# Kernel tuning notes

Hardware: AMD Instinct MI355X
Metric: run time of the kernel (lower is better)

## Reference

```python
import jax, jax.numpy as jnp
import numpy as np

N, DIM, HEADS, NS, KSP = 16384, 192, 6, 16, 16


def _forward(knn_idx, p, x, W_qkv, W_proj, b_proj, prop_W, prop_b, gA_W, gA_b, gB_W, gB_b,
             gC_W, gC_b, pos_W1, pos_b1, pos_gamma, pos_beta, pos_W2, pos_b2, kn,
             de_W1, de_b1, de_W2, de_b2, kp_W, kp_b, fus_W, fus_b):
    n, d = x.shape
    ns = knn_idx.shape[1]
    D = d // HEADS
    scale = D ** -0.5
    knn_xyz = p[knn_idx]                                  # [n,ns,3] irregular gather
    p_r = knn_xyz - p[:, None, :]                         # relative coords
    x_knn = x[knn_idx]                                    # [n,ns,d] irregular gather
    # PropagateLayer: rel-pos conditioned neighbor message + residual
    msg = jax.nn.relu(jnp.concatenate([x_knn, p_r], -1) @ prop_W + prop_b)
    x = x + msg.mean(1)
    # local polar representation
    dist_r = jnp.sqrt(jnp.sum(p_r * p_r, -1, keepdims=True) + 1e-12)   # [n,ns,1]
    geo_rep = jnp.concatenate([p_r, knn_xyz, jnp.broadcast_to(p[:, None, :], p_r.shape)], -1).mean(1)  # [n,9]
    geo_dis = dist_r.max(1)                               # [n,1]
    vol = (dist_r.mean() / (dist_r.max() + 1e-8)).reshape(1, 1)
    geo_rep = geo_rep @ gA_W + gA_b
    geo_dis = geo_dis @ gB_W + gB_b
    vol = vol @ gC_W + gC_b                               # [1,d] broadcast over n
    # keypoint distance features + attention pooling (KeyPointAttention)
    dist = jnp.sqrt(jnp.sum((p[:, None, :] - kn[None, :, :]) ** 2, -1) + 1e-12)  # [n,KSP]
    df = jax.nn.relu(dist[..., None] @ de_W1 + de_b1) @ de_W2 + de_b2            # [n,KSP,d]
    sc = jax.nn.softmax(df @ kp_W + kp_b, axis=1)
    dist_feat = (sc * df).sum(1)                          # [n,d]
    # FeatureFusion
    x = (x + geo_rep + geo_dis + vol + dist_feat) @ fus_W + fus_b
    # QueryGroup(local=True): window features + intra-window pairwise rel coords
    wx = x[knn_idx]                                       # [n,ns,d] irregular gather
    pos = (knn_xyz[:, None, :, :] - knn_xyz[:, :, None, :]).reshape(n, ns, ns * 3)  # [n,ns,48]

    def posi(i):  # Linear -> BatchNorm1d(dim) over (batch, window) -> ReLU -> Linear
        h = pos @ pos_W1[i] + pos_b1[i]                   # [n,ns,d]
        mu = h.mean((0, 1))
        var = h.var((0, 1))
        h = (h - mu) * jax.lax.rsqrt(var + 1e-5) * pos_gamma[i] + pos_beta[i]
        return jax.nn.relu(h) @ pos_W2[i] + pos_b2[i]

    pq, pk, pv = posi(0), posi(1), posi(2)
    q, k, v = jnp.split(wx @ W_qkv, 3, -1)

    def heads(t):
        return t.reshape(n, ns, HEADS, D).transpose(0, 2, 1, 3)  # [n,h,ns,D]

    q, k, v, pq, pk, pv = map(heads, (q, k, v, pq, pk, pv))
    dots = (jnp.einsum('nhid,nhjd->nhij', q, k)
            + jnp.einsum('nhid,nhjd->nhij', q, pq)
            + jnp.einsum('nhid,nhjd->nhij', k, pk))      # fused positional bias scores
    attn = jax.nn.softmax(dots * scale, -1)
    out = jnp.einsum('nhij,nhjd->nhid', attn, v + pv)
    out = out.transpose(0, 2, 1, 3).reshape(n, ns, d)[:, 0, :]   # take window center
    return out @ W_proj + b_proj


def setup_inputs() -> dict:
    key = jax.random.key(0)
    ks = jax.random.split(key, 20)
    d, s = DIM, 0.05
    rn = lambda i, shape: jax.random.normal(ks[i], shape, dtype=jnp.float32)
    return {
        'p': rn(0, (N, 3)),
        'x': rn(1, (N, d)),
        'knn_idx': jax.random.randint(ks[2], (N, NS), 0, N),
        'W_qkv': rn(3, (d, 3 * d)) * s,
        'W_proj': rn(4, (d, d)) * s,
        'b_proj': jnp.zeros((d,)),
        'prop_W': rn(5, (d + 3, d)) * s,
        'prop_b': jnp.zeros((d,)),
        'gA_W': rn(6, (9, d)) * s, 'gA_b': jnp.zeros((d,)),
        'gB_W': rn(7, (1, d)) * s, 'gB_b': jnp.zeros((d,)),
        'gC_W': rn(8, (1, d)) * s, 'gC_b': jnp.zeros((d,)),
        'pos_W1': rn(9, (3, NS * 3, d)) * s, 'pos_b1': jnp.zeros((3, d)),
        'pos_gamma': jnp.ones((3, d)), 'pos_beta': jnp.zeros((3, d)),
        'pos_W2': rn(10, (3, d, d)) * s, 'pos_b2': jnp.zeros((3, d)),
        'kn': rn(11, (KSP, 3)),
        'de_W1': rn(12, (1, d // 4)) * s, 'de_b1': jnp.zeros((d // 4,)),
        'de_W2': rn(13, (d // 4, d)) * s, 'de_b2': jnp.zeros((d,)),
        'kp_W': rn(14, (d, 1)) * s, 'kp_b': jnp.zeros((1,)),
        'fus_W': rn(15, (d, d)) * s, 'fus_b': jnp.zeros((d,)),
    }


def reference(p, x, knn_idx, W_qkv, W_proj, b_proj, prop_W, prop_b, gA_W, gA_b, gB_W, gB_b,
              gC_W, gC_b, pos_W1, pos_b1, pos_gamma, pos_beta, pos_W2, pos_b2, kn,
              de_W1, de_b1, de_W2, de_b2, kp_W, kp_b, fus_W, fus_b):
    return _forward(knn_idx, p, x, W_qkv, W_proj, b_proj, prop_W, prop_b, gA_W, gA_b,
                    gB_W, gB_b, gC_W, gC_b, pos_W1, pos_b1, pos_gamma, pos_beta,
                    pos_W2, pos_b2, kn, de_W1, de_b1, de_W2, de_b2, kp_W, kp_b, fus_W, fus_b)
```

## Files before the change

kernel.cpp:

```cpp
#include <hip/hip_runtime.h>
#include <math.h>

#define NP 16384
#define DD 192
#define NS 16
#define KSPN 16
#define MTOT (NP*NS)

typedef unsigned short ushort_t;
typedef __attribute__((ext_vector_type(8))) short short8;
typedef __attribute__((ext_vector_type(4))) float f32x4;

__device__ __forceinline__ ushort_t f2bf(float f) {
    union { float f; unsigned int u; } v; v.f = f;
    return (ushort_t)((v.u + 0x7FFFu + ((v.u >> 16) & 1u)) >> 16);
}
__device__ __forceinline__ float bf2f(ushort_t u) {
    return __uint_as_float(((unsigned int)u) << 16);
}

#define WS_KNN   0
#define WS_PR    (WS_KNN + NP*48)
#define WS_GEO9  (WS_PR + MTOT*3)
#define WS_GDIS  (WS_GEO9 + NP*9)
#define WS_STATS (WS_GDIS + NP)
#define WS_VOLV  (WS_STATS + 2512)
#define WS_AB    (WS_VOLV + DD)
#define WS_X1    (WS_AB + 1152)
#define WS_U     (WS_X1 + NP*DD)
#define WS_X2    (WS_U + NP*DD)
#define WS_QKV   (WS_X2 + NP*DD)
#define WS_SC    (WS_QKV + NP*576)
#define WS_ATTN  (WS_SC + NP*DD)
#define WS_W2T   (WS_ATTN + NP*96)
#define WS_PROPWT (WS_W2T + 36864)
#define WS_QKVT  (WS_PROPWT + 18432)
#define WS_FUSWT (WS_QKVT + 55296)
#define WS_PROJWT (WS_FUSWT + 18432)
#define WS_W1T   (WS_PROJWT + 18432)
#define WS_DEW2T (WS_W1T + 18432)
#define WS_XB    WS_SC
#define WS_UB    WS_ATTN
#define WS_X2B   WS_X2
#define WS_CTRB  WS_U

__global__ __launch_bounds__(256) void k_init(float* __restrict__ ws) {
    int t = blockIdx.x * 256 + threadIdx.x;
    if (t < 2512) ws[WS_STATS + t] = 0.f;
}

__global__ __launch_bounds__(256) void k_w2t(const float* __restrict__ posW2,
                                             float* __restrict__ ws) {
    int e = blockIdx.x*256 + threadIdx.x;
    int c = e / DD, kk = e - c*DD;
    ws[WS_W2T + e] = posW2[(size_t)(2*DD + kk)*DD + c];
}

__global__ __launch_bounds__(256) void k_prep(
    const float* __restrict__ propW, const float* __restrict__ Wqkv,
    const float* __restrict__ fusW, const float* __restrict__ Wproj,
    const float* __restrict__ posW1, const float* __restrict__ deW2,
    float* __restrict__ ws)
{
    int e = blockIdx.x*256 + threadIdx.x;
    ushort_t* pwt = (ushort_t*)(ws + WS_PROPWT);
    ushort_t* qkt = (ushort_t*)(ws + WS_QKVT);
    ushort_t* fwt = (ushort_t*)(ws + WS_FUSWT);
    ushort_t* pjt = (ushort_t*)(ws + WS_PROJWT);
    ushort_t* w1t = (ushort_t*)(ws + WS_W1T);
    ushort_t* dwt = (ushort_t*)(ws + WS_DEW2T);
    if (e < 36864) {
        int n = e/192, k = e - n*192;
        pwt[e] = f2bf(propW[(size_t)k*192 + n]);
    } else if (e < 147456) {
        int r = e - 36864; int n = r/192, k = r - n*192;
        qkt[r] = f2bf(Wqkv[(size_t)k*576 + n]);
    } else if (e < 184320) {
        int r = e - 147456; int n = r/192, k = r - n*192;
        fwt[r] = f2bf(fusW[(size_t)k*192 + n]);
    } else if (e < 221184) {
        int r = e - 184320; int n = r/192, k = r - n*192;
        pjt[r] = f2bf(Wproj[(size_t)k*192 + n]);
    } else if (e < 258048) {
        int r = e - 221184;
        int i = r / 12288, rem = r - i*12288;
        int n = rem / 64, k = rem - n*64;
        w1t[r] = (k < 48) ? f2bf(posW1[(size_t)(i*48 + k)*DD + n]) : (ushort_t)0;
    } else if (e < 270336) {
        int r = e - 258048;
        int n = r / 64, k = r - n*64;
        dwt[r] = (k < 48) ? f2bf(deW2[(size_t)k*DD + n]) : (ushort_t)0;
    }
}

__global__ __launch_bounds__(256) void k_castx(const float* __restrict__ x,
                                               float* __restrict__ ws) {
    int e = blockIdx.x*256 + threadIdx.x;
    ((ushort_t*)(ws + WS_XB))[e] = f2bf(x[e]);
}

__global__ __launch_bounds__(256) void k1a_geom(
    const float* __restrict__ p, const int* __restrict__ knn,
    float* __restrict__ ws)
{
    __shared__ float red[32];
    const int t = threadIdx.x;
    const int w = t >> 4, u = t & 15;
    const int n = blockIdx.x*16 + w;
    const int idx = knn[n*NS + u];
    const float X0 = p[idx*3+0], X1 = p[idx*3+1], X2 = p[idx*3+2];
    const float pn0 = p[n*3+0], pn1 = p[n*3+1], pn2 = p[n*3+2];
    ws[WS_KNN + (size_t)n*48 + u*3 + 0] = X0;
    ws[WS_KNN + (size_t)n*48 + u*3 + 1] = X1;
    ws[WS_KNN + (size_t)n*48 + u*3 + 2] = X2;
    const float dx = X0-pn0, dy = X1-pn1, dz = X2-pn2;
    ws[WS_PR + (size_t)(n*NS+u)*3 + 0] = dx;
    ws[WS_PR + (size_t)(n*NS+u)*3 + 1] = dy;
    ws[WS_PR + (size_t)(n*NS+u)*3 + 2] = dz;
    const float dist = sqrtf(dx*dx + dy*dy + dz*dz + 1e-12f);
    float dmx = dist, dsm = dist, S0 = X0, S1 = X1, S2 = X2;
    #pragma unroll
    for (int off = 1; off < 16; off <<= 1) {
        dmx = fmaxf(dmx, __shfl_xor(dmx, off, 16));
        dsm += __shfl_xor(dsm, off, 16);
        S0 += __shfl_xor(S0, off, 16);
        S1 += __shfl_xor(S1, off, 16);
        S2 += __shfl_xor(S2, off, 16);
    }
    if (u == 0) {
        ws[WS_GDIS + n] = dmx;
        float m0 = S0*(1.f/16.f), m1 = S1*(1.f/16.f), m2 = S2*(1.f/16.f);
        float* g = ws + WS_GEO9 + (size_t)n*9;
        g[0] = m0-pn0; g[1] = m1-pn1; g[2] = m2-pn2;
        g[3] = m0; g[4] = m1; g[5] = m2;
        g[6] = pn0; g[7] = pn1; g[8] = pn2;
        red[w] = dsm; red[16+w] = dmx;
    }
    __syncthreads();
    if (t == 0) {
        float ds = 0.f, dm = 0.f;
        #pragma unroll
        for (int i = 0; i < 16; ++i) { ds += red[i]; dm = fmaxf(dm, red[16+i]); }
        atomicAdd(&ws[WS_STATS + 0], ds);
        atomicMax((int*)(ws + WS_STATS + 1), __float_as_int(dm));
    }
}

__global__ __launch_bounds__(256) void k1b_stats(float* __restrict__ ws)
{
    __shared__ float Xs[128][48];
    __shared__ float Ss[128][3];
    __shared__ float a3p[9][16];
    const int t = threadIdx.x;
    const int c0 = blockIdx.x * 128;
    for (int e = t; e < 1536; e += 256) {
        int r = e/12, q = e%12;
        *(float4*)&Xs[r][q*4] = *(const float4*)(ws + WS_KNN + (size_t)(c0+r)*48 + q*4);
    }
    __syncthreads();
    if (t < 128) {
        float s0 = 0.f, s1 = 0.f, s2 = 0.f;
        #pragma unroll
        for (int j = 0; j < 16; ++j) { s0 += Xs[t][3*j]; s1 += Xs[t][3*j+1]; s2 += Xs[t][3*j+2]; }
        Ss[t][0] = s0; Ss[t][1] = s1; Ss[t][2] = s2;
    }
    __syncthreads();
    {
        float acc[9];
        #pragma unroll
        for (int q = 0; q < 9; ++q) acc[q] = 0.f;
        for (int i = 0; i < 128; ++i) {
            int e = t;
            #pragma unroll
            for (int q = 0; q < 9; ++q) {
                int a = e/48, b = e%48;
                acc[q] += Xs[i][a] * Xs[i][b];
                e += 256;
            }
        }
        int e = t;
        #pragma unroll
        for (int q = 0; q < 9; ++q) { atomicAdd(&ws[WS_STATS + 50 + e], acc[q]); e += 256; }
    }
    if (t < 144) {
        int a = t/3, d = t%3;
        float s = 0.f;
        for (int i = 0; i < 128; ++i) s += Xs[i][a] * Ss[i][d];
        atomicAdd(&ws[WS_STATS + 2354 + t], s);
    }
    if (t < 144) {
        int q = t >> 4, part = t & 15;
        int d = q/3, e2 = q%3;
        float s = 0.f;
        for (int i = part*8; i < part*8 + 8; ++i) {
            #pragma unroll
            for (int j = 0; j < 16; ++j) s += Xs[i][3*j+d] * Xs[i][3*j+e2];
        }
        a3p[q][part] = s;
    }
    if (t < 48) {
        float s = 0.f;
        for (int i = 0; i < 128; ++i) s += Xs[i][t];
        atomicAdd(&ws[WS_STATS + 2 + t], s);
    }
    if (t < 3) {
        float s = 0.f;
        for (int i = 0; i < 128; ++i) s += Ss[i][t];
        atomicAdd(&ws[WS_STATS + 2507 + t], s);
    }
    __syncthreads();
    if (t < 9) {
        float s = 0.f;
        #pragma unroll
        for (int i = 0; i < 16; ++i) s += a3p[t][i];
        atomicAdd(&ws[WS_STATS + 2498 + t], s);
    }
}

__global__ __launch_bounds__(256) void k2_fold(
    const float* __restrict__ posW1, const float* __restrict__ posB1,
    const float* __restrict__ gamma, const float* __restrict__ beta,
    const float* __restrict__ gCW, const float* __restrict__ gCb,
    float* __restrict__ ws)
{
    __shared__ float M2n[48][48];
    __shared__ float pmean[48];
    __shared__ float Wc[48][193];
    const int t = threadIdx.x;
    const int i = blockIdx.x;
    for (int e = t; e < 2304; e += 256) {
        int a = e/48, b = e%48, ad = a%3, bd = b%3;
        float v = 16.f*ws[WS_STATS + 50 + e]
                - ws[WS_STATS + 2354 + a*3 + bd]
                - ws[WS_STATS + 2354 + b*3 + ad]
                + ws[WS_STATS + 2498 + ad*3 + bd];
        M2n[a][b] = v * (1.f/(float)MTOT);
    }
    if (t < 48) pmean[t] = (16.f*ws[WS_STATS + 2 + t] - ws[WS_STATS + 2507 + t%3])
                           * (1.f/(float)MTOT);
    if (t < DD) {
        for (int k = 0; k < 48; ++k) Wc[k][t] = posW1[(size_t)(i*48 + k)*DD + t];
    }
    __syncthreads();
    if (i == 0 && t < DD) {
        float dsum = ws[WS_STATS + 0];
        float dmax = __int_as_float(((const int*)(ws + WS_STATS))[1]);
        float vol = (dsum * (1.f/(float)MTOT)) / (dmax + 1e-8f);
        ws[WS_VOLV + t] = vol * gCW[t] + gCb[t];
    }
    if (t < DD) {
        float mu0 = 0.f;
        #pragma unroll 8
        for (int k = 0; k < 48; ++k) mu0 += pmean[k] * Wc[k][t];
        float e2 = 0.f;
        for (int a2 = 0; a2 < 48; ++a2) {
            float inner = 0.f;
            #pragma unroll 8
            for (int b2 = 0; b2 < 48; ++b2) inner += M2n[a2][b2] * Wc[b2][t];
            e2 += Wc[a2][t] * inner;
        }
        float var = fmaxf(e2 - mu0*mu0, 0.f);
        float as = rsqrtf(var + 1e-5f) * gamma[i*DD + t];
        ws[WS_AB + i*DD + t]       = as;
        ws[WS_AB + 576 + i*DD + t] = beta[i*DD + t] - mu0 * as;
    }
}

__global__ __launch_bounds__(256) void k_prop_mfma(
    const float* __restrict__ x, const int* __restrict__ knn,
    const float* __restrict__ propW, const float* __restrict__ propB,
    float* __restrict__ ws)
{
    __shared__ ushort_t As[64*40];
    __shared__ ushort_t Bs[192*40];
    __shared__ float prs[64*3];
    __shared__ float W3[3*192];
    __shared__ int idx64[64];
    const int t = threadIdx.x;
    const int mbase = blockIdx.x * 64;
    const ushort_t* xb = (const ushort_t*)(ws + WS_XB);
    const ushort_t* pwt = (const ushort_t*)(ws + WS_PROPWT);
    if (t < 64) idx64[t] = knn[mbase + t];
    for (int e = t; e < 576; e += 256) W3[e] = propW[(size_t)(192 + e/192)*DD + (e % 192)];
    for (int e = t; e < 192; e += 256) prs[e] = ws[WS_PR + (size_t)mbase*3 + e];
    const int wave = t >> 6, lane = t & 63, m = lane & 15, quad = lane >> 4;
    f32x4 acc[12];
    #pragma unroll
    for (int nt = 0; nt < 12; ++nt) acc[nt] = (f32x4){0.f,0.f,0.f,0.f};
    for (int ks = 0; ks < 6; ++ks) {
        const int k0 = ks*32;
        __syncthreads();
        {   int r = t >> 2, seg = t & 3;
            *(uint4*)&As[r*40 + seg*8] = *(const uint4*)(xb + (size_t)idx64[r]*192 + k0 + seg*8);
        }
        for (int e = t; e < 768; e += 256) {
            int n = e >> 2, seg = e & 3;
            *(uint4*)&Bs[n*40 + seg*8] = *(const uint4*)(pwt + (size_t)n*192 + k0 + seg*8);
        }
        __syncthreads();
        short8 a = *(const short8*)&As[(wave*16 + m)*40 + quad*8];
        #pragma unroll
        for (int nt = 0; nt < 12; ++nt) {
            short8 b = *(const short8*)&Bs[(nt*16 + m)*40 + quad*8];
            acc[nt] = __builtin_amdgcn_mfma_f32_16x16x32_bf16(a, b, acc[nt], 0, 0, 0);
        }
    }
    const int n = blockIdx.x*4 + wave;
    #pragma unroll
    for (int nt = 0; nt < 12; ++nt) {
        int col = nt*16 + m;
        float bv = propB[col];
        float w0 = W3[col], w1 = W3[192 + col], w2 = W3[384 + col];
        float s = 0.f;
        #pragma unroll
        for (int reg = 0; reg < 4; ++reg) {
            int j = wave*16 + quad*4 + reg;
            float v = acc[nt][reg] + prs[j*3+0]*w0 + prs[j*3+1]*w1 + prs[j*3+2]*w2 + bv;
            s += fmaxf(v, 0.f);
        }
        s += __shfl_xor(s, 16);
        s += __shfl_xor(s, 32);
        if (quad == 0)
            ws[WS_X1 + (size_t)n*DD + col] = x[(size_t)n*DD + col] + s * (1.f/16.f);
    }
}

__global__ __launch_bounds__(256) void gemm_mfma(
    const ushort_t* __restrict__ A, const ushort_t* __restrict__ Bt,
    const float* __restrict__ bias, float* __restrict__ Cf,
    ushort_t* __restrict__ Cb, int N)
{
    __shared__ ushort_t As[64*40];
    __shared__ ushort_t Bs[64*40];
    const int t = threadIdx.x;
    const int wave = t >> 6, lane = t & 63, m = lane & 15, quad = lane >> 4;
    const int rowBase = blockIdx.x * 64, colBase = blockIdx.y * 64;
    f32x4 acc[4];
    #pragma unroll
    for (int nt = 0; nt < 4; ++nt) acc[nt] = (f32x4){0.f,0.f,0.f,0.f};
    for (int ks = 0; ks < 6; ++ks) {
        __syncthreads();
        {   int r = t >> 2, seg = t & 3;
            *(uint4*)&As[r*40 + seg*8] = *(const uint4*)(A + (size_t)(rowBase + r)*192 + ks*32 + seg*8);
            *(uint4*)&Bs[r*40 + seg*8] = *(const uint4*)(Bt + (size_t)(colBase + r)*192 + ks*32 + seg*8);
        }
        __syncthreads();
        short8 a = *(const short8*)&As[(wave*16 + m)*40 + quad*8];
        #pragma unroll
        for (int nt = 0; nt < 4; ++nt) {
            short8 b = *(const short8*)&Bs[(nt*16 + m)*40 + quad*8];
            acc[nt] = __builtin_amdgcn_mfma_f32_16x16x32_bf16(a, b, acc[nt], 0, 0, 0);
        }
    }
    #pragma unroll
    for (int nt = 0; nt < 4; ++nt) {
        int col = colBase + nt*16 + m;
        float bv = bias ? bias[col] : 0.f;
        #pragma unroll
        for (int reg = 0; reg < 4; ++reg) {
            int row = rowBase + wave*16 + quad*4 + reg;
            float v = acc[nt][reg] + bv;
            if (Cf) Cf[(size_t)row*N + col] = v;
            else    Cb[(size_t)row*N + col] = f2bf(v);
        }
    }
}

__global__ __launch_bounds__(256) void k3a(
    const float* __restrict__ p, const float* __restrict__ kn,
    const float* __restrict__ deW1, const float* __restrict__ deB1,
    const float* __restrict__ deB2, const float* __restrict__ kpW,
    const float* __restrict__ gAW, const float* __restrict__ gAb,
    const float* __restrict__ gBW, const float* __restrict__ gBb,
    float* __restrict__ ws)
{
    __shared__ ushort_t fb[128*72];
    __shared__ float kds[8][16];
    __shared__ float w1s[48], b1s[48];
    __shared__ float dfeat[8][192];
    ushort_t* ub = (ushort_t*)(ws + WS_UB);
    const int t = threadIdx.x;
    const int nb = blockIdx.x * 8;
    if (t < 48) { w1s[t] = deW1[t]; b1s[t] = deB1[t]; }
    if (t < 128) {
        int w = t >> 4, kp = t & 15;
        float dx = p[(nb+w)*3+0]-kn[kp*3+0];
        float dy = p[(nb+w)*3+1]-kn[kp*3+1];
        float dz = p[(nb+w)*3+2]-kn[kp*3+2];
        kds[w][kp] = sqrtf(dx*dx + dy*dy + dz*dz + 1e-12f);
    }
    __syncthreads();
    for (int e = t; e < 128*64; e += 256) {
        int j = e >> 6, k = e & 63;
        float v = (k < 48) ? fmaxf(kds[j>>4][j&15]*w1s[k] + b1s[k], 0.f) : 0.f;
        fb[j*72 + k] = f2bf(v);
    }
    __syncthreads();
    const int wave = t >> 6, lane = t & 63, m = lane & 15, quad = lane >> 4;
    const ushort_t* dwt = (const ushort_t*)(ws + WS_DEW2T);
    short8 afr[2][2];
    #pragma unroll
    for (int mt = 0; mt < 2; ++mt)
        #pragma unroll
        for (int ks = 0; ks < 2; ++ks)
            afr[mt][ks] = *(const short8*)&fb[((wave*2 + mt)*16 + m)*72 + ks*32 + quad*8];
    float df[2][12][4];
    float sc[2][4];
    #pragma unroll
    for (int mt = 0; mt < 2; ++mt)
        #pragma unroll
        for (int reg = 0; reg < 4; ++reg) sc[mt][reg] = 0.f;
    for (int nt = 0; nt < 12; ++nt) {
        f32x4 acc0 = (f32x4){0.f,0.f,0.f,0.f};
        f32x4 acc1 = (f32x4){0.f,0.f,0.f,0.f};
        #pragma unroll
        for (int ks = 0; ks < 2; ++ks) {
            short8 b = *(const short8*)(dwt + ((size_t)(nt*16 + m)*64 + ks*32 + quad*8));
            acc0 = __builtin_amdgcn_mfma_f32_16x16x32_bf16(afr[0][ks], b, acc0, 0, 0, 0);
            acc1 = __builtin_amdgcn_mfma_f32_16x16x32_bf16(afr[1][ks], b, acc1, 0, 0, 0);
        }
        int col = nt*16 + m;
        float b2 = deB2[col], kw = kpW[col];
        #pragma unroll
        for (int reg = 0; reg < 4; ++reg) {
            float d0 = acc0[reg] + b2, d1 = acc1[reg] + b2;
            df[0][nt][reg] = d0; df[1][nt][reg] = d1;
            sc[0][reg] += d0*kw; sc[1][reg] += d1*kw;
        }
    }
    #pragma unroll
    for (int mt = 0; mt < 2; ++mt)
        #pragma unroll
        for (int reg = 0; reg < 4; ++reg) {
            float v = sc[mt][reg];
            v += __shfl_xor(v, 1, 16); v += __shfl_xor(v, 2, 16);
            v += __shfl_xor(v, 4, 16); v += __shfl_xor(v, 8, 16);
            sc[mt][reg] = v;
        }
    float wgt[2][4];
    #pragma unroll
    for (int mt = 0; mt < 2; ++mt) {
        float mx = fmaxf(fmaxf(sc[mt][0], sc[mt][1]), fmaxf(sc[mt][2], sc[mt][3]));
        mx = fmaxf(mx, __shfl_xor(mx, 16));
        mx = fmaxf(mx, __shfl_xor(mx, 32));
        float sm = 0.f;
        #pragma unroll
        for (int reg = 0; reg < 4; ++reg) { wgt[mt][reg] = expf(sc[mt][reg] - mx); sm += wgt[mt][reg]; }
        sm += __shfl_xor(sm, 16);
        sm += __shfl_xor(sm, 32);
        float inv = 1.f / sm;
        #pragma unroll
        for (int reg = 0; reg < 4; ++reg) wgt[mt][reg] *= inv;
    }
    for (int nt = 0; nt < 12; ++nt) {
        int col = nt*16 + m;
        #pragma unroll
        for (int mt = 0; mt < 2; ++mt) {
            float s = 0.f;
            #pragma unroll
            for (int reg = 0; reg < 4; ++reg) s += wgt[mt][reg] * df[mt][nt][reg];
            s += __shfl_xor(s, 16);
            s += __shfl_xor(s, 32);
            if (quad == 0) dfeat[wave*2 + mt][col] = s;
        }
    }
    __syncthreads();
    if (t < DD) {
        for (int w = 0; w < 8; ++w) {
            int n = nb + w;
            float uval = ws[WS_X1 + (size_t)n*DD + t] + gAb[t] + gBb[t]
                       + ws[WS_VOLV + t] + dfeat[w][t];
            uval += ws[WS_GDIS + n] * gBW[t];
            #pragma unroll
            for (int kk = 0; kk < 9; ++kk) uval += ws[WS_GEO9 + (size_t)n*9 + kk] * gAW[kk*DD + t];
            ub[(size_t)n*DD + t] = f2bf(uval);
        }
    }
}

__global__ __launch_bounds__(256) void k_attn_fused(
    const int* __restrict__ knn,
    const float* __restrict__ posW2, const float* __restrict__ posB2,
    float* __restrict__ ws)
{
    __shared__ ushort_t posb[128*72];
    __shared__ float rqs[8*6*192];
    __shared__ float qk[8*192];
    __shared__ float scb[8*192];
    __shared__ float dqk[8*96];
    __shared__ float attns[8*96];
    __shared__ float Xl[8][48];
    __shared__ int idxs[128];
    const int t = threadIdx.x;
    const int nb = blockIdx.x * 8;
    ushort_t* ctrb = (ushort_t*)(ws + WS_CTRB);
    const ushort_t* qkvb = (const ushort_t*)(ws + WS_QKV);
    if (t < 128) idxs[t] = knn[(nb + (t >> 4))*NS + (t & 15)];
    for (int e = t; e < 384; e += 256) {
        int w = e/48, k = e%48;
        Xl[w][k] = ws[WS_KNN + (size_t)(nb+w)*48 + k];
    }
    __syncthreads();
    for (int e = t; e < 128*64; e += 256) {
        int j = e >> 6, k = e & 63;
        int w = j >> 4, jl = j & 15;
        float v = (k < 48) ? (Xl[w][k] - Xl[w][jl*3 + (k % 3)]) : 0.f;
        posb[j*72 + k] = f2bf(v);
    }
    const int wave = t >> 6, lane = t & 63, m = lane & 15, quad = lane >> 4;
    const ushort_t* w1t = (const ushort_t*)(ws + WS_W1T);
    for (int i = 0; i < 2; ++i) {
        __syncthreads();
        for (int e = t; e < 8*192; e += 256) {
            int w = e/192, c = e%192;
            qk[e] = bf2f(qkvb[(size_t)idxs[w*16]*576 + i*192 + c]);
        }
        __syncthreads();
        if (t < 192) {
            const float* Wrow = posW2 + (size_t)i*DD*DD + (size_t)t*DD;
            for (int h = 0; h < 6; ++h) {
                float4 wr[8];
                #pragma unroll
                for (int q = 0; q < 8; ++q) wr[q] = *(const float4*)(Wrow + h*32 + q*4);
                float a[8];
                #pragma unroll
                for (int w = 0; w < 8; ++w) a[w] = 0.f;
                #pragma unroll
                for (int q = 0; q < 8; ++q) {
                    #pragma unroll
                    for (int d = 0; d < 4; ++d) {
                        float wv = (&wr[q].x)[d];
                        int c = h*32 + q*4 + d;
                        #pragma unroll
                        for (int w = 0; w < 8; ++w) a[w] += wv * qk[w*192 + c];
                    }
                }
                #pragma unroll
                for (int w = 0; w < 8; ++w) rqs[(w*6 + h)*192 + t] = a[w];
            }
        }
        __syncthreads();
        short8 afr[2][2];
        #pragma unroll
        for (int mt = 0; mt < 2; ++mt)
            #pragma unroll
            for (int ks = 0; ks < 2; ++ks)
                afr[mt][ks] = *(const short8*)&posb[((wave*2 + mt)*16 + m)*72 + ks*32 + quad*8];
        float s[48];
        #pragma unroll
        for (int e = 0; e < 48; ++e) s[e] = 0.f;
        for (int nt = 0; nt < 12; ++nt) {
            f32x4 acc0 = (f32x4){0.f,0.f,0.f,0.f};
            f32x4 acc1 = (f32x4){0.f,0.f,0.f,0.f};
            #pragma unroll
            for (int ks = 0; ks < 2; ++ks) {
                short8 b = *(const short8*)(w1t + ((size_t)(i*192 + nt*16 + m)*64 + ks*32 + quad*8));
                acc0 = __builtin_amdgcn_mfma_f32_16x16x32_bf16(afr[0][ks], b, acc0, 0, 0, 0);
                acc1 = __builtin_amdgcn_mfma_f32_16x16x32_bf16(afr[1][ks], b, acc1, 0, 0, 0);
            }
            int kk = nt*16 + m;
            float as = ws[WS_AB + i*DD + kk];
            float bb = ws[WS_AB + 576 + i*DD + kk];
            float h0[4], h1[4];
            #pragma unroll
            for (int reg = 0; reg < 4; ++reg) {
                h0[reg] = fmaxf(acc0[reg]*as + bb, 0.f);
                h1[reg] = fmaxf(acc1[reg]*as + bb, 0.f);
            }
            #pragma unroll
            for (int h = 0; h < 6; ++h) {
                float r0 = rqs[((wave*2 + 0)*6 + h)*192 + kk];
                float r1 = rqs[((wave*2 + 1)*6 + h)*192 + kk];
                #pragma unroll
                for (int reg = 0; reg < 4; ++reg) {
                    s[reg*6 + h]      += h0[reg]*r0;
                    s[24 + reg*6 + h] += h1[reg]*r1;
                }
            }
        }
        #pragma unroll
        for (int e = 0; e < 48; ++e) {
            float v = s[e];
            v += __shfl_xor(v, 1, 16); v += __shfl_xor(v, 2, 16);
            v += __shfl_xor(v, 4, 16); v += __shfl_xor(v, 8, 16);
            s[e] = v;
        }
        if (m == 0) {
            #pragma unroll
            for (int mt = 0; mt < 2; ++mt)
                #pragma unroll
                for (int reg = 0; reg < 4; ++reg) {
                    int w = wave*2 + mt, j = quad*4 + reg;
                    #pragma unroll
                    for (int h = 0; h < 6; ++h)
                        scb[w*192 + i*96 + h*16 + j] = s[mt*24 + reg*6 + h];
                }
        }
    }
    {
        const int w = t >> 5, r = t & 31, j = r >> 1, half = r & 1;
        const ushort_t* krow = qkvb + (size_t)idxs[w*16 + j]*576 + 192 + half*96;
        const ushort_t* qrow = qkvb + (size_t)idxs[w*16]*576 + half*96;
        float hd[3] = {0.f, 0.f, 0.f};
        #pragma unroll
        for (int q = 0; q < 12; ++q) {
            uint4 kv = *(const uint4*)(krow + q*8);
            uint4 qv = *(const uint4*)(qrow + q*8);
            float sv = 0.f;
            #pragma unroll
            for (int d = 0; d < 4; ++d) {
                unsigned int ku = (&kv.x)[d], qu = (&qv.x)[d];
                sv += __uint_as_float(ku << 16) * __uint_as_float(qu << 16);
                sv += __uint_as_float(ku & 0xffff0000u) * __uint_as_float(qu & 0xffff0000u);
            }
            hd[q >> 2] += sv;
        }
        dqk[w*96 + (half*3+0)*16 + j] = hd[0];
        dqk[w*96 + (half*3+1)*16 + j] = hd[1];
        dqk[w*96 + (half*3+2)*16 + j] = hd[2];
    }
    __syncthreads();
    {
        const float scale = 0.17677669529663687f;
        #pragma unroll
        for (int c = 0; c < 3; ++c) {
            int e = c*256 + t;
            int row = e >> 4, j = e & 15, w = row / 6, h = row % 6;
            float z = (dqk[e] + scb[w*192 + h*16 + j] + scb[w*192 + 96 + h*16 + j]) * scale;
            float mx = z;
            #pragma unroll
            for (int off = 1; off < 16; off <<= 1) mx = fmaxf(mx, __shfl_xor(mx, off, 16));
            float ex = expf(z - mx);
            float sm = ex;
            #pragma unroll
            for (int off = 1; off < 16; off <<= 1) sm += __shfl_xor(sm, off, 16);
            attns[w*96 + h*16 + j] = ex / sm;
        }
    }
    __syncthreads();
    float ctr1[8];
    if (t < DD) {
        const int h = t >> 5;
        #pragma unroll
        for (int w = 0; w < 8; ++w) {
            float sv = 0.f;
            #pragma unroll
            for (int j = 0; j < NS; ++j)
                sv += attns[w*96 + h*16 + j] * bf2f(qkvb[(size_t)idxs[w*16 + j]*576 + 384 + t]);
            ctr1[w] = sv;
        }
    }
    {
        float* wsum = rqs;
        const int w0 = wave*2, w1 = wave*2 + 1;
        short8 afr[2][2];
        #pragma unroll
        for (int mt = 0; mt < 2; ++mt)
            #pragma unroll
            for (int ks = 0; ks < 2; ++ks)
                afr[mt][ks] = *(const short8*)&posb[((wave*2 + mt)*16 + m)*72 + ks*32 + quad*8];
        for (int nt = 0; nt < 12; ++nt) {
            f32x4 acc0 = (f32x4){0.f,0.f,0.f,0.f};
            f32x4 acc1 = (f32x4){0.f,0.f,0.f,0.f};
            #pragma unroll
            for (int ks = 0; ks < 2; ++ks) {
                short8 b = *(const short8*)(w1t + ((size_t)(2*192 + nt*16 + m)*64 + ks*32 + quad*8));
                acc0 = __builtin_amdgcn_mfma_f32_16x16x32_bf16(afr[0][ks], b, acc0, 0, 0, 0);
                acc1 = __builtin_amdgcn_mfma_f32_16x16x32_bf16(afr[1][ks], b, acc1, 0, 0, 0);
            }
            int kk = nt*16 + m;
            float as = ws[WS_AB + 2*DD + kk];
            float bb = ws[WS_AB + 576 + 2*DD + kk];
            float h0[4], h1[4];
            #pragma unroll
            for (int reg = 0; reg < 4; ++reg) {
                h0[reg] = fmaxf(acc0[reg]*as + bb, 0.f);
                h1[reg] = fmaxf(acc1[reg]*as + bb, 0.f);
            }
            #pragma unroll
            for (int h = 0; h < 6; ++h) {
                float p0 = 0.f, p1 = 0.f;
                #pragma unroll
                for (int reg = 0; reg < 4; ++reg) {
                    int j = quad*4 + reg;
                    p0 += attns[w0*96 + h*16 + j] * h0[reg];
                    p1 += attns[w1*96 + h*16 + j] * h1[reg];
                }
                p0 += __shfl_xor(p0, 16); p0 += __shfl_xor(p0, 32);
                p1 += __shfl_xor(p1, 16); p1 += __shfl_xor(p1, 32);
                if (quad == 0) {
                    wsum[(w0*6 + h)*192 + kk] = p0;
                    wsum[(w1*6 + h)*192 + kk] = p1;
                }
            }
        }
    }
    __syncthreads();
    if (t < DD) {
        const float* wsum = rqs;
        const int h = t >> 5;
        float pvacc[8];
        #pragma unroll
        for (int w = 0; w < 8; ++w) pvacc[w] = 0.f;
        const float* wrow = ws + WS_W2T + (size_t)t*DD;
        for (int k4 = 0; k4 < 48; ++k4) {
            float4 wv = *(const float4*)(wrow + k4*4);
            #pragma unroll
            for (int w = 0; w < 8; ++w) {
                const float* av = &wsum[(w*6 + h)*192 + k4*4];
                pvacc[w] += av[0]*wv.x + av[1]*wv.y + av[2]*wv.z + av[3]*wv.w;
            }
        }
        float b2 = posB2[2*DD + t];
        #pragma unroll
        for (int w = 0; w < 8; ++w)
            ctrb[(size_t)(nb+w)*DD + t] = f2bf(ctr1[w] + pvacc[w] + b2);
    }
}

extern "C" void kernel_launch(void* const* d_in, const int* in_sizes, int n_in,
                              void* d_out, int out_size, void* d_ws, size_t ws_size,
                              hipStream_t stream)
{
    const float* p     = (const float*)d_in[0];
    const float* x     = (const float*)d_in[1];
    const int*   knn   = (const int*)  d_in[2];
    const float* Wqkv  = (const float*)d_in[3];
    const float* Wproj = (const float*)d_in[4];
    const float* bproj = (const float*)d_in[5];
    const float* propW = (const float*)d_in[6];
    const float* propB = (const float*)d_in[7];
    const float* gAW   = (const float*)d_in[8];
    const float* gAb   = (const float*)d_in[9];
    const float* gBW   = (const float*)d_in[10];
    const float* gBb   = (const float*)d_in[11];
    const float* gCW   = (const float*)d_in[12];
    const float* gCb   = (const float*)d_in[13];
    const float* posW1 = (const float*)d_in[14];
    const float* posB1 = (const float*)d_in[15];
    const float* gamma = (const float*)d_in[16];
    const float* beta  = (const float*)d_in[17];
    const float* posW2 = (const float*)d_in[18];
    const float* posB2 = (const float*)d_in[19];
    const float* kn    = (const float*)d_in[20];
    const float* deW1  = (const float*)d_in[21];
    const float* deB1  = (const float*)d_in[22];
    const float* deW2  = (const float*)d_in[23];
    const float* deB2  = (const float*)d_in[24];
    const float* kpW   = (const float*)d_in[25];
    const float* kpB   = (const float*)d_in[26];
    const float* fusW  = (const float*)d_in[27];
    const float* fusB  = (const float*)d_in[28];
    float* ws   = (float*)d_ws;
    float* outp = (float*)d_out;
    (void)kpB;

    hipLaunchKernelGGL(k_init, dim3(10), dim3(256), 0, stream, ws);
    hipLaunchKernelGGL(k_w2t, dim3(144), dim3(256), 0, stream, posW2, ws);
    hipLaunchKernelGGL(k_prep, dim3(1056), dim3(256), 0, stream,
                       propW, Wqkv, fusW, Wproj, posW1, deW2, ws);
    hipLaunchKernelGGL(k_castx, dim3(NP*DD/256), dim3(256), 0, stream, x, ws);
    hipLaunchKernelGGL(k1a_geom, dim3(NP/16), dim3(256), 0, stream, p, knn, ws);
    hipLaunchKernelGGL(k1b_stats, dim3(NP/128), dim3(256), 0, stream, ws);
    hipLaunchKernelGGL(k2_fold, dim3(3), dim3(256), 0, stream,
                       posW1, posB1, gamma, beta, gCW, gCb, ws);
    hipLaunchKernelGGL(k_prop_mfma, dim3(MTOT/64), dim3(256), 0, stream,
                       x, knn, propW, propB, ws);
    hipLaunchKernelGGL(k3a, dim3(NP/8), dim3(256), 0, stream,
                       p, kn, deW1, deB1, deB2, kpW, gAW, gAb, gBW, gBb, ws);
    hipLaunchKernelGGL(gemm_mfma, dim3(NP/64, 3), dim3(256), 0, stream,
                       (const ushort_t*)(ws + WS_UB), (const ushort_t*)(ws + WS_FUSWT),
                       fusB, (float*)nullptr, (ushort_t*)(ws + WS_X2B), DD);
    hipLaunchKernelGGL(gemm_mfma, dim3(NP/64, 9), dim3(256), 0, stream,
                       (const ushort_t*)(ws + WS_X2B), (const ushort_t*)(ws + WS_QKVT),
                       (const float*)nullptr, (float*)nullptr,
                       (ushort_t*)(ws + WS_QKV), 576);
    hipLaunchKernelGGL(k_attn_fused, dim3(NP/8), dim3(256), 0, stream,
                       knn, posW2, posB2, ws);
    hipLaunchKernelGGL(gemm_mfma, dim3(NP/64, 3), dim3(256), 0, stream,
                       (const ushort_t*)(ws + WS_CTRB), (const ushort_t*)(ws + WS_PROJWT),
                       bproj, outp, (ushort_t*)nullptr, DD);
}
```

Baseline: 663.9 us.

## Shrink shared memory in attention kernel to raise occupancy

Removes the shared-memory posb staging buffer and builds the MFMA A-fragments of relative positions directly in registers from Xl, once per block instead of reloading them per pass. Stores the rqs/wsum intermediate in bf16 instead of fp32, halving that shared buffer, and adds a launch bound of 4 blocks per SM. Together these cut LDS use so more blocks can be resident, at the cost of extra bf16 rounding on the intermediates and more register pressure from keeping the fragments live across loops.

```diff
diff --git a/kernel.cpp b/kernel.cpp
--- a/kernel.cpp
+++ b/kernel.cpp
@@ -478,13 +478,12 @@
     }
 }
 
-__global__ __launch_bounds__(256) void k_attn_fused(
+__global__ __launch_bounds__(256, 4) void k_attn_fused(
     const int* __restrict__ knn,
     const float* __restrict__ posW2, const float* __restrict__ posB2,
     float* __restrict__ ws)
 {
-    __shared__ ushort_t posb[128*72];
-    __shared__ float rqs[8*6*192];
+    __shared__ ushort_t rqs[8*6*192];
     __shared__ float qk[8*192];
     __shared__ float scb[8*192];
     __shared__ float dqk[8*96];
@@ -501,13 +500,23 @@
         Xl[w][k] = ws[WS_KNN + (size_t)(nb+w)*48 + k];
     }
     __syncthreads();
-    for (int e = t; e < 128*64; e += 256) {
-        int j = e >> 6, k = e & 63;
-        int w = j >> 4, jl = j & 15;
-        float v = (k < 48) ? (Xl[w][k] - Xl[w][jl*3 + (k % 3)]) : 0.f;
-        posb[j*72 + k] = f2bf(v);
-    }
     const int wave = t >> 6, lane = t & 63, m = lane & 15, quad = lane >> 4;
+    short8 afr[2][2];
+    #pragma unroll
+    for (int mt = 0; mt < 2; ++mt) {
+        const int w = wave*2 + mt;
+        #pragma unroll
+        for (int ks = 0; ks < 2; ++ks) {
+            short8 v;
+            #pragma unroll
+            for (int e = 0; e < 8; ++e) {
+                const int k = ks*32 + quad*8 + e;
+                float f = (k < 48) ? (Xl[w][k] - Xl[w][m*3 + (k % 3)]) : 0.f;
+                v[e] = (short)f2bf(f);
+            }
+            afr[mt][ks] = v;
+        }
+    }
     const ushort_t* w1t = (const ushort_t*)(ws + WS_W1T);
     for (int i = 0; i < 2; ++i) {
         __syncthreads();
@@ -536,16 +545,10 @@
                     }
                 }
                 #pragma unroll
-                for (int w = 0; w < 8; ++w) rqs[(w*6 + h)*192 + t] = a[w];
+                for (int w = 0; w < 8; ++w) rqs[(w*6 + h)*192 + t] = f2bf(a[w]);
             }
         }
         __syncthreads();
-        short8 afr[2][2];
-        #pragma unroll
-        for (int mt = 0; mt < 2; ++mt)
-            #pragma unroll
-            for (int ks = 0; ks < 2; ++ks)
-                afr[mt][ks] = *(const short8*)&posb[((wave*2 + mt)*16 + m)*72 + ks*32 + quad*8];
         float s[48];
         #pragma unroll
         for (int e = 0; e < 48; ++e) s[e] = 0.f;
@@ -569,8 +572,8 @@
             }
             #pragma unroll
             for (int h = 0; h < 6; ++h) {
-                float r0 = rqs[((wave*2 + 0)*6 + h)*192 + kk];
-                float r1 = rqs[((wave*2 + 1)*6 + h)*192 + kk];
+                float r0 = bf2f(rqs[((wave*2 + 0)*6 + h)*192 + kk]);
+                float r1 = bf2f(rqs[((wave*2 + 1)*6 + h)*192 + kk]);
                 #pragma unroll
                 for (int reg = 0; reg < 4; ++reg) {
                     s[reg*6 + h]      += h0[reg]*r0;
@@ -651,14 +654,8 @@
         }
     }
     {
-        float* wsum = rqs;
+        ushort_t* wsum = rqs;
         const int w0 = wave*2, w1 = wave*2 + 1;
-        short8 afr[2][2];
-        #pragma unroll
-        for (int mt = 0; mt < 2; ++mt)
-            #pragma unroll
-            for (int ks = 0; ks < 2; ++ks)
-                afr[mt][ks] = *(const short8*)&posb[((wave*2 + mt)*16 + m)*72 + ks*32 + quad*8];
         for (int nt = 0; nt < 12; ++nt) {
             f32x4 acc0 = (f32x4){0.f,0.f,0.f,0.f};
             f32x4 acc1 = (f32x4){0.f,0.f,0.f,0.f};
@@ -689,15 +686,15 @@
                 p0 += __shfl_xor(p0, 16); p0 += __shfl_xor(p0, 32);
                 p1 += __shfl_xor(p1, 16); p1 += __shfl_xor(p1, 32);
                 if (quad == 0) {
-                    wsum[(w0*6 + h)*192 + kk] = p0;
-                    wsum[(w1*6 + h)*192 + kk] = p1;
+                    wsum[(w0*6 + h)*192 + kk] = f2bf(p0);
+                    wsum[(w1*6 + h)*192 + kk] = f2bf(p1);
                 }
             }
         }
     }
     __syncthreads();
     if (t < DD) {
-        const float* wsum = rqs;
+        const ushort_t* wsum = rqs;
         const int h = t >> 5;
         float pvacc[8];
         #pragma unroll
@@ -707,8 +704,9 @@
             float4 wv = *(const float4*)(wrow + k4*4);
             #pragma unroll
             for (int w = 0; w < 8; ++w) {
-                const float* av = &wsum[(w*6 + h)*192 + k4*4];
-                pvacc[w] += av[0]*wv.x + av[1]*wv.y + av[2]*wv.z + av[3]*wv.w;
+                const ushort_t* av = &wsum[(w*6 + h)*192 + k4*4];
+                pvacc[w] += bf2f(av[0])*wv.x + bf2f(av[1])*wv.y
+                          + bf2f(av[2])*wv.z + bf2f(av[3])*wv.w;
             }
         }
         float b2 = posB2[2*DD + t];
```

Result: faster. 611.1 us (-7.9%).
